# Performance work log

Measured on AMD Instinct MI355X. Metric: run time of the kernel, lower is better.

The kernel has to match this reference:

```python
import jax, jax.numpy as jnp
import numpy as np

NUM_HEADS = 4

def setup_inputs() -> dict:
    key = jax.random.key(0)
    ks = jax.random.split(key, 8)
    B, C, H, W = 4, 256, 128, 128
    Cq = C // 8  # query/key channels
    x  = jax.random.normal(ks[0], (B, C, H, W), dtype=jnp.float32)
    Wq = jax.random.normal(ks[1], (Cq, C), dtype=jnp.float32) * 0.05
    bq = jax.random.normal(ks[2], (Cq,),  dtype=jnp.float32) * 0.01
    Wk = jax.random.normal(ks[3], (Cq, C), dtype=jnp.float32) * 0.05
    bk = jax.random.normal(ks[4], (Cq,),  dtype=jnp.float32) * 0.01
    Wv = jax.random.normal(ks[5], (C, C),  dtype=jnp.float32) * 0.05
    bv = jax.random.normal(ks[6], (C,),   dtype=jnp.float32) * 0.01
    # torch init is zeros; use a nonzero value so the attention path contributes
    gamma = jnp.array([0.5], dtype=jnp.float32)
    return {"x": x, "Wq": Wq, "bq": bq, "Wk": Wk, "bk": bk, "Wv": Wv, "bv": bv, "gamma": gamma}

def _conv1x1(x, Wm, b):
    # 1x1 conv == per-pixel linear map over channels
    return jnp.einsum('bchw,oc->bohw', x, Wm) + b[None, :, None, None]

def reference(x, Wq, bq, Wk, bk, Wv, bv, gamma):
    B, C, H, W = x.shape
    nh = NUM_HEADS
    # project, then fold heads into batch: (B*nh, c_head, H, W)
    q = _conv1x1(x, Wq, bq).reshape(B * nh, -1, H, W)
    k = _conv1x1(x, Wk, bk).reshape(B * nh, -1, H, W)
    v = _conv1x1(x, Wv, bv).reshape(B * nh, -1, H, W)
    # horizontal (row-wise) attention over W: energy [BH, H, W, W]
    e_h = jnp.einsum('bchw,bchv->bhwv', q, k)
    a_h = jax.nn.softmax(e_h, axis=-1)
    o_h = jnp.einsum('bhwv,bchv->bchw', a_h, v)  # (BH, cv, H, W)
    # vertical (column-wise) attention over H: energy [BH, W, H, H]
    e_v = jnp.einsum('bchw,bcgw->bwhg', q, k)
    a_v = jax.nn.softmax(e_v, axis=-1)
    # original permutes back as (BH, cv, W, H); requires H == W to add
    o_v = jnp.einsum('bwhg,bcgw->bcwh', a_v, v)
    attn = (o_h + o_v).reshape(B, C, H, W)
    return gamma * attn + x
```

## Files before the change

kernel.cpp:

```cpp
#include <hip/hip_runtime.h>

#define HW 16384

typedef __attribute__((ext_vector_type(8))) short short8;
typedef __attribute__((ext_vector_type(16))) float floatx16;

__device__ inline unsigned short f2bf(float f) {
    unsigned u = __builtin_bit_cast(unsigned, f);
    u = (u + 0x7FFFu + ((u >> 16) & 1u)) >> 16;
    return (unsigned short)u;
}

__device__ inline unsigned pack_bf_trunc(float lo, float hi) {
    return __builtin_amdgcn_perm(__builtin_bit_cast(unsigned, hi),
                                 __builtin_bit_cast(unsigned, lo), 0x07060302u);
}

__global__ __launch_bounds__(256) void castW_kernel(
    const float* __restrict__ Wq, const float* __restrict__ Wk,
    const float* __restrict__ Wv, unsigned short* __restrict__ Wb)
{
    int idx4 = blockIdx.x * 256 + threadIdx.x;
    int e0 = idx4 * 4;
    int row = e0 >> 8, col = e0 & 255;
    const float* src = (row < 32) ? (Wq + row * 256 + col)
                     : (row < 64) ? (Wk + (row - 32) * 256 + col)
                                  : (Wv + (row - 64) * 256 + col);
    float4 v = *(const float4*)src;
    uint2 pk;
    pk.x = f2bf(v.x) | ((unsigned)f2bf(v.y) << 16);
    pk.y = f2bf(v.z) | ((unsigned)f2bf(v.w) << 16);
    *(uint2*)&Wb[e0] = pk;
}

__global__ __launch_bounds__(256) void cast_xt_kernel(
    const float* __restrict__ x, unsigned short* __restrict__ xt)
{
    __shared__ unsigned short T[64][66];
    const int tid = threadIdx.x;
    const int p0 = blockIdx.x * 64;
    const int c0 = blockIdx.y * 64;
    const int b  = blockIdx.z;
    #pragma unroll
    for (int i = 0; i < 4; i++) {
        int e = i * 256 + tid;
        int c = e >> 4, seg = e & 15;
        float4 v = *(const float4*)&x[((b * 256 + c0 + c) << 14) + p0 + seg * 4];
        ((unsigned*)&T[c][seg * 4])[0] = f2bf(v.x) | ((unsigned)f2bf(v.y) << 16);
        ((unsigned*)&T[c][seg * 4])[1] = f2bf(v.z) | ((unsigned)f2bf(v.w) << 16);
    }
    __syncthreads();
    #pragma unroll
    for (int i = 0; i < 2; i++) {
        int e = i * 256 + tid;
        int p = e >> 3, cs = e & 7;
        unsigned short t[8];
        #pragma unroll
        for (int j = 0; j < 8; j++) t[j] = T[cs * 8 + j][p];
        uint4 pk;
        pk.x = t[0] | ((unsigned)t[1] << 16);
        pk.y = t[2] | ((unsigned)t[3] << 16);
        pk.z = t[4] | ((unsigned)t[5] << 16);
        pk.w = t[6] | ((unsigned)t[7] << 16);
        *(uint4*)&xt[(((b << 14) + p0 + p) << 8) + c0 + cs * 8] = pk;
    }
}

__global__ __launch_bounds__(256, 3) void proj_mfma_kernel(
    const unsigned short* __restrict__ Wb, const unsigned short* __restrict__ xt,
    const float* __restrict__ bq, const float* __restrict__ bk,
    const float* __restrict__ bv,
    unsigned short* __restrict__ qb, unsigned short* __restrict__ kb,
    unsigned short* __restrict__ vb)
{
    __shared__ __align__(16) unsigned short As[64 * 64];
    __shared__ __align__(16) unsigned short Bs[256 * 64];
    __shared__ float biasS[64];
    const int tid = threadIdx.x;
    const int p0  = blockIdx.x * 256;
    const int oc0 = blockIdx.y * 64;
    const int b   = blockIdx.z;
    const int w = tid >> 6, lr = tid & 31, lh = (tid & 63) >> 5;

    if (tid < 64) biasS[tid] = (oc0 == 0) ? ((tid < 32) ? bq[tid] : bk[tid - 32])
                                          : bv[oc0 - 64 + tid];

    floatx16 z16 = {0,0,0,0,0,0,0,0,0,0,0,0,0,0,0,0};
    floatx16 acc[2][2] = {{z16, z16}, {z16, z16}};
    const int bpx = (b << 14) + p0;

    for (int kc = 0; kc < 256; kc += 64) {
        if (kc) __syncthreads();
        #pragma unroll
        for (int i = 0; i < 2; i++) {
            int e = i * 256 + tid;
            int row = e >> 3, seg = e & 7, cp = seg ^ (row & 7);
            *(uint4*)&As[row * 64 + cp * 8] =
                *(const uint4*)&Wb[(oc0 + row) * 256 + kc + seg * 8];
        }
        #pragma unroll
        for (int i = 0; i < 8; i++) {
            int e = i * 256 + tid;
            int row = e >> 3, seg = e & 7, cp = seg ^ (row & 7);
            *(uint4*)&Bs[row * 64 + cp * 8] =
                *(const uint4*)&xt[((bpx + row) << 8) + kc + seg * 8];
        }
        __syncthreads();
        #pragma unroll
        for (int ks = 0; ks < 4; ks++) {
            int c = 2 * ks + lh;
            int cx = (c ^ (lr & 7)) * 8;
            short8 af0 = *(const short8*)&As[lr * 64 + cx];
            short8 af1 = *(const short8*)&As[(32 + lr) * 64 + cx];
            short8 bf0 = *(const short8*)&Bs[(64 * w + lr) * 64 + cx];
            short8 bf1 = *(const short8*)&Bs[(64 * w + 32 + lr) * 64 + cx];
            acc[0][0] = __builtin_amdgcn_mfma_f32_32x32x16_bf16(af0, bf0, acc[0][0], 0, 0, 0);
            acc[0][1] = __builtin_amdgcn_mfma_f32_32x32x16_bf16(af0, bf1, acc[0][1], 0, 0, 0);
            acc[1][0] = __builtin_amdgcn_mfma_f32_32x32x16_bf16(af1, bf0, acc[1][0], 0, 0, 0);
            acc[1][1] = __builtin_amdgcn_mfma_f32_32x32x16_bf16(af1, bf1, acc[1][1], 0, 0, 0);
        }
    }

    __syncthreads();
    if (oc0 == 0) {
        unsigned short* Cq = Bs;
        #pragma unroll
        for (int i = 0; i < 2; i++) {
            #pragma unroll
            for (int j = 0; j < 2; j++) {
                int px = 64 * w + 32 * j + lr;
                #pragma unroll
                for (int g = 0; g < 4; g++) {
                    float v0 = acc[i][j][4*g+0] + biasS[32*i + 8*g + 4*lh + 0];
                    float v1 = acc[i][j][4*g+1] + biasS[32*i + 8*g + 4*lh + 1];
                    float v2 = acc[i][j][4*g+2] + biasS[32*i + 8*g + 4*lh + 2];
                    float v3 = acc[i][j][4*g+3] + biasS[32*i + 8*g + 4*lh + 3];
                    uint2 u; u.x = pack_bf_trunc(v0, v1); u.y = pack_bf_trunc(v2, v3);
                    int cp = (4 * i + g) ^ (px & 7);
                    *(uint2*)&Cq[px * 64 + cp * 8 + 4 * lh] = u;
                }
            }
        }
        __syncthreads();
        #pragma unroll
        for (int i = 0; i < 8; i++) {
            int px = tid;
            int cp = i ^ (px & 7);
            uint4 val = *(const uint4*)&Cq[px * 64 + cp * 8];
            if (i < 4) *(uint4*)&qb[(unsigned)((b * 4 + i)     * HW + p0 + px) * 8] = val;
            else       *(uint4*)&kb[(unsigned)((b * 4 + i - 4) * HW + p0 + px) * 8] = val;
        }
    } else {
        unsigned short* Cv = Bs;
        #pragma unroll
        for (int i = 0; i < 2; i++) {
            #pragma unroll
            for (int j = 0; j < 2; j++) {
                int px = 64 * w + 32 * j + lr;
                #pragma unroll
                for (int reg = 0; reg < 16; reg++) {
                    int oc = 32 * i + (reg & 3) + 8 * (reg >> 2) + 4 * lh;
                    float v = acc[i][j][reg] + biasS[oc];
                    int cp = (px >> 3) ^ (oc & 31);
                    Cv[oc * 256 + cp * 8 + (px & 7)] =
                        (unsigned short)(__builtin_bit_cast(unsigned, v) >> 16);
                }
            }
        }
        __syncthreads();
        #pragma unroll
        for (int i = 0; i < 8; i++) {
            int u = i * 256 + tid;
            int oc = u >> 5, seg = u & 31;
            int cp = seg ^ (oc & 31);
            uint4 val = *(const uint4*)&Cv[oc * 256 + cp * 8];
            *(uint4*)&vb[(unsigned)(b * 256 + oc0 - 64 + oc) * HW + p0 + seg * 8] = val;
        }
    }
}

__global__ __launch_bounds__(256) void tqk_kernel(
    const unsigned short* __restrict__ qb, const unsigned short* __restrict__ kb,
    unsigned short* __restrict__ qt, unsigned short* __restrict__ kt)
{
    __shared__ uint4 t[32][33];
    const int plane = blockIdx.y;
    const int tile  = blockIdx.x;
    const int tx = tile & 3, ty = tile >> 2;
    const uint4* src = (const uint4*)(plane < 16 ? qb : kb) + (plane & 15) * HW;
    uint4*       dst = (uint4*)(plane < 16 ? qt : kt) + (plane & 15) * HW;
    const int c = threadIdx.x & 31, r0 = threadIdx.x >> 5;
    #pragma unroll
    for (int i = 0; i < 4; i++) {
        int r = r0 + i * 8;
        t[r][c] = src[(ty * 32 + r) * 128 + tx * 32 + c];
    }
    __syncthreads();
    #pragma unroll
    for (int i = 0; i < 4; i++) {
        int r = r0 + i * 8;
        dst[(tx * 32 + r) * 128 + ty * 32 + c] = t[c][r];
    }
}

__global__ __launch_bounds__(256) void tv_kernel(
    const unsigned short* __restrict__ vb, unsigned short* __restrict__ vt)
{
    __shared__ unsigned short T[64][66];
    const int plane = blockIdx.y;
    const int tile  = blockIdx.x;
    const int tx = tile & 1, ty = tile >> 1;
    const unsigned* src = (const unsigned*)(vb + plane * HW);
    unsigned*       dst = (unsigned*)(vt + plane * HW);
    const int tid = threadIdx.x;
    #pragma unroll
    for (int i = 0; i < 8; i++) {
        int e = i * 256 + tid;
        int r = e >> 5, cp = e & 31;
        *(unsigned*)&T[r][2 * cp] = src[(ty * 64 + r) * 64 + tx * 32 + cp];
    }
    __syncthreads();
    #pragma unroll
    for (int i = 0; i < 8; i++) {
        int e = i * 256 + tid;
        int c = e >> 5, rp = e & 31;
        unsigned lo = T[2 * rp][c], hi = T[2 * rp + 1][c];
        dst[(tx * 64 + c) * 64 + ty * 32 + rp] = lo | (hi << 16);
    }
}

__global__ __launch_bounds__(256, 3) void attn_kernel(
    const unsigned short* __restrict__ qb, const unsigned short* __restrict__ kb,
    const unsigned short* __restrict__ vb,
    const unsigned short* __restrict__ qt, const unsigned short* __restrict__ kt,
    const unsigned short* __restrict__ vt,
    const float* __restrict__ xin, const float* __restrict__ gamma,
    float* __restrict__ out)
{
    __shared__ __align__(16) unsigned short Vs[64 * 128];
    __shared__ __align__(16) unsigned short Ps[128 * 128];
    __shared__ float red[4][128];

    const int tid = threadIdx.x;
    const int y = blockIdx.x, bh = blockIdx.y;
    const int w = tid >> 6, l = tid & 63, lr = l & 31, lh = l >> 5;
    const float L2E = 1.4426950408889634f;

    floatx16 z16 = {0,0,0,0,0,0,0,0,0,0,0,0,0,0,0,0};
    floatx16 o0 = z16, o1 = z16;
    short8 z8 = {0,0,0,0,0,0,0,0};

    for (int stage = 0; stage < 2; stage++) {
        const unsigned short* qsrc = (stage ? qt : qb) + (bh * 128 + y) * 1024;
        const unsigned short* ksrc = (stage ? kt : kb) + (bh * 128 + y) * 1024;
        const unsigned short* vsrc = stage ? vt : vb;
        if (stage) __syncthreads();
        #pragma unroll
        for (int i = 0; i < 4; i++) {
            int e = i * 256 + tid;
            int ch = e >> 4, sg = e & 15;
            int sgp = sg ^ (ch & 15);
            *(uint4*)&Vs[ch * 128 + sgp * 8] =
                *(const uint4*)(vsrc + (bh * 64 + ch) * HW + y * 128 + sg * 8);
        }
        short8 af = z8;
        short8 bf[4] = {z8, z8, z8, z8};
        if (lh == 0) {
            af = *(const short8*)(ksrc + (32 * w + lr) * 8);
            #pragma unroll
            for (int nt = 0; nt < 4; nt++)
                bf[nt] = *(const short8*)(qsrc + (32 * nt + lr) * 8);
        }
        floatx16 et[4];
        #pragma unroll
        for (int nt = 0; nt < 4; nt++)
            et[nt] = __builtin_amdgcn_mfma_f32_32x32x16_bf16(af, bf[nt], z16, 0, 0, 0);

        #pragma unroll
        for (int nt = 0; nt < 4; nt++) {
            float s = 0.f;
            #pragma unroll
            for (int r = 0; r < 16; r++) {
                float p = exp2f(et[nt][r] * L2E);
                et[nt][r] = p;
                s += p;
            }
            s += __shfl_xor(s, 32);
            if (lh == 0) red[w][32 * nt + lr] = s;
        }
        __syncthreads();
        float rl[4];
        #pragma unroll
        for (int nt = 0; nt < 4; nt++) {
            int q = 32 * nt + lr;
            rl[nt] = 1.0f / (red[0][q] + red[1][q] + red[2][q] + red[3][q]);
        }
        #pragma unroll
        for (int nt = 0; nt < 4; nt++) {
            int row = 32 * nt + lr;
            #pragma unroll
            for (int g = 0; g < 4; g++) {
                uint2 u;
                u.x = pack_bf_trunc(et[nt][4*g+0] * rl[nt], et[nt][4*g+1] * rl[nt]);
                u.y = pack_bf_trunc(et[nt][4*g+2] * rl[nt], et[nt][4*g+3] * rl[nt]);
                int cp = (4 * w + g) ^ (lr & 15);
                *(uint2*)&Ps[row * 128 + cp * 8 + 4 * lh] = u;
            }
        }
        __syncthreads();
        #pragma unroll
        for (int ks = 0; ks < 8; ks++) {
            int cp = ((2 * ks + lh) ^ (lr & 15)) * 8;
            short8 pf = *(const short8*)&Ps[(32 * w + lr) * 128 + cp];
            short8 v0 = *(const short8*)&Vs[lr * 128 + cp];
            short8 v1 = *(const short8*)&Vs[(32 + lr) * 128 + cp];
            o0 = __builtin_amdgcn_mfma_f32_32x32x16_bf16(v0, pf, o0, 0, 0, 0);
            o1 = __builtin_amdgcn_mfma_f32_32x32x16_bf16(v1, pf, o1, 0, 0, 0);
        }
    }

    const float g = gamma[0];
    const int xq = 32 * w + lr;
    #pragma unroll
    for (int reg = 0; reg < 16; reg++) {
        int ch = (reg & 3) + 8 * (reg >> 2) + 4 * lh;
        int idx0 = (bh * 64 + ch) * HW + y * 128 + xq;
        int idx1 = (bh * 64 + 32 + ch) * HW + y * 128 + xq;
        out[idx0] = g * o0[reg] + xin[idx0];
        out[idx1] = g * o1[reg] + xin[idx1];
    }
}

extern "C" void kernel_launch(void* const* d_in, const int* in_sizes, int n_in,
                              void* d_out, int out_size, void* d_ws, size_t ws_size,
                              hipStream_t stream) {
    const float* x     = (const float*)d_in[0];
    const float* Wq    = (const float*)d_in[1];
    const float* bq    = (const float*)d_in[2];
    const float* Wk    = (const float*)d_in[3];
    const float* bk    = (const float*)d_in[4];
    const float* Wv    = (const float*)d_in[5];
    const float* bv    = (const float*)d_in[6];
    const float* gamma = (const float*)d_in[7];
    float* out = (float*)d_out;

    unsigned short* Wb   = (unsigned short*)d_ws;
    unsigned short* qb16 = Wb + 320 * 256;
    unsigned short* kb16 = qb16 + 16 * HW * 8;
    unsigned short* qt16 = kb16 + 16 * HW * 8;
    unsigned short* kt16 = qt16 + 16 * HW * 8;
    unsigned short* vb16 = kt16 + 16 * HW * 8;
    unsigned short* vt16 = vb16 + 1024 * HW;
    unsigned short* xt = (unsigned short*)d_out;

    castW_kernel<<<dim3(80), 256, 0, stream>>>(Wq, Wk, Wv, Wb);
    cast_xt_kernel<<<dim3(256, 4, 4), 256, 0, stream>>>(x, xt);
    proj_mfma_kernel<<<dim3(64, 5, 4), 256, 0, stream>>>(Wb, xt, bq, bk, bv, qb16, kb16, vb16);
    tqk_kernel<<<dim3(16, 32), 256, 0, stream>>>(qb16, kb16, qt16, kt16);
    tv_kernel<<<dim3(4, 1024), 256, 0, stream>>>(vb16, vt16);
    attn_kernel<<<dim3(128, 16), 256, 0, stream>>>(qb16, kb16, vb16, qt16, kt16, vt16, x, gamma, out);
}
```

Baseline: 202.4 us.

## Restructure projection to stage x tile once, make attention register-resident

The projection kernel now loads a full 128-pixel x 256-channel tile of x into shared memory once. It loops over all five output-channel groups, reading weights directly from global memory, instead of launching a separate block per group that reloads x. The attention kernel computes energies transposed so each wave holds its own query columns. It builds the P operand in registers through lane shuffles instead of writing to shared memory, and drops the cross-wave softmax reduction barrier by deferring normalization (rescaling stage-0 output by the sum ratio). Both V tiles are preloaded up front. This trades shared-memory traffic and barriers for more registers, and changes occupancy targets on both kernels.

```diff
diff --git a/kernel.cpp b/kernel.cpp
--- a/kernel.cpp
+++ b/kernel.cpp
@@ -66,115 +66,103 @@
     }
 }
 
-__global__ __launch_bounds__(256, 3) void proj_mfma_kernel(
+__global__ __launch_bounds__(256, 2) void proj_mfma_kernel(
     const unsigned short* __restrict__ Wb, const unsigned short* __restrict__ xt,
     const float* __restrict__ bq, const float* __restrict__ bk,
     const float* __restrict__ bv,
     unsigned short* __restrict__ qb, unsigned short* __restrict__ kb,
     unsigned short* __restrict__ vb)
 {
-    __shared__ __align__(16) unsigned short As[64 * 64];
-    __shared__ __align__(16) unsigned short Bs[256 * 64];
-    __shared__ float biasS[64];
+    __shared__ __align__(16) unsigned short Bs[128 * 256];
+    __shared__ __align__(16) unsigned short Cs[32 * 128];
+    __shared__ float biasS[320];
     const int tid = threadIdx.x;
-    const int p0  = blockIdx.x * 256;
-    const int oc0 = blockIdx.y * 64;
-    const int b   = blockIdx.z;
+    const int p0  = blockIdx.x * 128;
+    const int b   = blockIdx.y;
     const int w = tid >> 6, lr = tid & 31, lh = (tid & 63) >> 5;
 
-    if (tid < 64) biasS[tid] = (oc0 == 0) ? ((tid < 32) ? bq[tid] : bk[tid - 32])
-                                          : bv[oc0 - 64 + tid];
+    if (tid < 64) biasS[tid] = (tid < 32) ? bq[tid] : bk[tid - 32];
+    biasS[64 + tid] = bv[tid];
+
+    const int bpx = (b << 14) + p0;
+    #pragma unroll
+    for (int i = 0; i < 16; i++) {
+        int e = i * 256 + tid;
+        int row = e >> 5, c = e & 31, cp = c ^ (row & 7);
+        *(uint4*)&Bs[row * 256 + cp * 8] =
+            *(const uint4*)&xt[(bpx + row) * 256 + c * 8];
+    }
+    __syncthreads();
 
     floatx16 z16 = {0,0,0,0,0,0,0,0,0,0,0,0,0,0,0,0};
-    floatx16 acc[2][2] = {{z16, z16}, {z16, z16}};
-    const int bpx = (b << 14) + p0;
-
-    for (int kc = 0; kc < 256; kc += 64) {
-        if (kc) __syncthreads();
-        #pragma unroll
-        for (int i = 0; i < 2; i++) {
-            int e = i * 256 + tid;
-            int row = e >> 3, seg = e & 7, cp = seg ^ (row & 7);
-            *(uint4*)&As[row * 64 + cp * 8] =
-                *(const uint4*)&Wb[(oc0 + row) * 256 + kc + seg * 8];
-        }
-        #pragma unroll
-        for (int i = 0; i < 8; i++) {
-            int e = i * 256 + tid;
-            int row = e >> 3, seg = e & 7, cp = seg ^ (row & 7);
-            *(uint4*)&Bs[row * 64 + cp * 8] =
-                *(const uint4*)&xt[((bpx + row) << 8) + kc + seg * 8];
-        }
-        __syncthreads();
-        #pragma unroll
-        for (int ks = 0; ks < 4; ks++) {
-            int c = 2 * ks + lh;
-            int cx = (c ^ (lr & 7)) * 8;
-            short8 af0 = *(const short8*)&As[lr * 64 + cx];
-            short8 af1 = *(const short8*)&As[(32 + lr) * 64 + cx];
-            short8 bf0 = *(const short8*)&Bs[(64 * w + lr) * 64 + cx];
-            short8 bf1 = *(const short8*)&Bs[(64 * w + 32 + lr) * 64 + cx];
-            acc[0][0] = __builtin_amdgcn_mfma_f32_32x32x16_bf16(af0, bf0, acc[0][0], 0, 0, 0);
-            acc[0][1] = __builtin_amdgcn_mfma_f32_32x32x16_bf16(af0, bf1, acc[0][1], 0, 0, 0);
-            acc[1][0] = __builtin_amdgcn_mfma_f32_32x32x16_bf16(af1, bf0, acc[1][0], 0, 0, 0);
-            acc[1][1] = __builtin_amdgcn_mfma_f32_32x32x16_bf16(af1, bf1, acc[1][1], 0, 0, 0);
-        }
-    }
-
-    __syncthreads();
-    if (oc0 == 0) {
-        unsigned short* Cq = Bs;
-        #pragma unroll
-        for (int i = 0; i < 2; i++) {
-            #pragma unroll
-            for (int j = 0; j < 2; j++) {
-                int px = 64 * w + 32 * j + lr;
+    const int brow = 32 * w + lr;
+
+    for (int ocg = 0; ocg < 5; ocg++) {
+        const int oc0 = ocg * 64;
+        floatx16 acc[2] = {z16, z16};
+        const unsigned short* wrow0 = Wb + (oc0 + lr) * 256 + 8 * lh;
+        const unsigned short* wrow1 = Wb + (oc0 + 32 + lr) * 256 + 8 * lh;
+        #pragma unroll
+        for (int ks = 0; ks < 16; ks++) {
+            short8 af0 = *(const short8*)(wrow0 + 16 * ks);
+            short8 af1 = *(const short8*)(wrow1 + 16 * ks);
+            int cpk = ((2 * ks + lh) ^ (brow & 7)) * 8;
+            short8 bfr = *(const short8*)&Bs[brow * 256 + cpk];
+            acc[0] = __builtin_amdgcn_mfma_f32_32x32x16_bf16(af0, bfr, acc[0], 0, 0, 0);
+            acc[1] = __builtin_amdgcn_mfma_f32_32x32x16_bf16(af1, bfr, acc[1], 0, 0, 0);
+        }
+
+        if (ocg == 0) {
+            #pragma unroll
+            for (int i = 0; i < 2; i++) {
+                int px = 32 * w + lr;
                 #pragma unroll
                 for (int g = 0; g < 4; g++) {
-                    float v0 = acc[i][j][4*g+0] + biasS[32*i + 8*g + 4*lh + 0];
-                    float v1 = acc[i][j][4*g+1] + biasS[32*i + 8*g + 4*lh + 1];
-                    float v2 = acc[i][j][4*g+2] + biasS[32*i + 8*g + 4*lh + 2];
-                    float v3 = acc[i][j][4*g+3] + biasS[32*i + 8*g + 4*lh + 3];
+                    float v0 = acc[i][4*g+0] + biasS[32*i + 8*g + 4*lh + 0];
+                    float v1 = acc[i][4*g+1] + biasS[32*i + 8*g + 4*lh + 1];
+                    float v2 = acc[i][4*g+2] + biasS[32*i + 8*g + 4*lh + 2];
+                    float v3 = acc[i][4*g+3] + biasS[32*i + 8*g + 4*lh + 3];
                     uint2 u; u.x = pack_bf_trunc(v0, v1); u.y = pack_bf_trunc(v2, v3);
-                    int cp = (4 * i + g) ^ (px & 7);
-                    *(uint2*)&Cq[px * 64 + cp * 8 + 4 * lh] = u;
+                    int cp = g ^ (px & 3);
+                    *(uint2*)&Cs[px * 32 + cp * 8 + 4 * lh] = u;
                 }
+                __syncthreads();
+                #pragma unroll
+                for (int i2 = 0; i2 < 2; i2++) {
+                    int u4 = i2 * 256 + tid;
+                    int hl = u4 >> 7, px2 = u4 & 127;
+                    int cp = hl ^ (px2 & 3);
+                    uint4 val = *(const uint4*)&Cs[px2 * 32 + cp * 8];
+                    unsigned off = (unsigned)((b * 4 + hl) * HW + p0 + px2) * 8;
+                    if (i == 0) *(uint4*)&qb[off] = val;
+                    else        *(uint4*)&kb[off] = val;
+                }
+                __syncthreads();
             }
-        }
-        __syncthreads();
-        #pragma unroll
-        for (int i = 0; i < 8; i++) {
-            int px = tid;
-            int cp = i ^ (px & 7);
-            uint4 val = *(const uint4*)&Cq[px * 64 + cp * 8];
-            if (i < 4) *(uint4*)&qb[(unsigned)((b * 4 + i)     * HW + p0 + px) * 8] = val;
-            else       *(uint4*)&kb[(unsigned)((b * 4 + i - 4) * HW + p0 + px) * 8] = val;
-        }
-    } else {
-        unsigned short* Cv = Bs;
-        #pragma unroll
-        for (int i = 0; i < 2; i++) {
-            #pragma unroll
-            for (int j = 0; j < 2; j++) {
-                int px = 64 * w + 32 * j + lr;
+        } else {
+            #pragma unroll
+            for (int i = 0; i < 2; i++) {
+                int px = 32 * w + lr;
                 #pragma unroll
                 for (int reg = 0; reg < 16; reg++) {
-                    int oc = 32 * i + (reg & 3) + 8 * (reg >> 2) + 4 * lh;
-                    float v = acc[i][j][reg] + biasS[oc];
-                    int cp = (px >> 3) ^ (oc & 31);
-                    Cv[oc * 256 + cp * 8 + (px & 7)] =
+                    int m = (reg & 3) + 8 * (reg >> 2) + 4 * lh;
+                    float v = acc[i][reg] + biasS[oc0 + 32 * i + m];
+                    int cp = (px >> 3) ^ (m & 15);
+                    Cs[m * 128 + cp * 8 + (px & 7)] =
                         (unsigned short)(__builtin_bit_cast(unsigned, v) >> 16);
                 }
+                __syncthreads();
+                #pragma unroll
+                for (int i2 = 0; i2 < 2; i2++) {
+                    int u4 = i2 * 256 + tid;
+                    int m = u4 >> 4, seg = u4 & 15;
+                    int cp = seg ^ (m & 15);
+                    uint4 val = *(const uint4*)&Cs[m * 128 + cp * 8];
+                    *(uint4*)&vb[(unsigned)((b * 256 + oc0 - 64 + 32 * i + m) * HW
+                                            + p0 + seg * 8)] = val;
+                }
+                __syncthreads();
             }
-        }
-        __syncthreads();
-        #pragma unroll
-        for (int i = 0; i < 8; i++) {
-            int u = i * 256 + tid;
-            int oc = u >> 5, seg = u & 31;
-            int cp = seg ^ (oc & 31);
-            uint4 val = *(const uint4*)&Cv[oc * 256 + cp * 8];
-            *(uint4*)&vb[(unsigned)(b * 256 + oc0 - 64 + oc) * HW + p0 + seg * 8] = val;
         }
     }
 }
@@ -229,7 +217,7 @@
     }
 }
 
-__global__ __launch_bounds__(256, 3) void attn_kernel(
+__global__ __launch_bounds__(256, 4) void attn_kernel(
     const unsigned short* __restrict__ qb, const unsigned short* __restrict__ kb,
     const unsigned short* __restrict__ vb,
     const unsigned short* __restrict__ qt, const unsigned short* __restrict__ kt,
@@ -237,97 +225,96 @@
     const float* __restrict__ xin, const float* __restrict__ gamma,
     float* __restrict__ out)
 {
-    __shared__ __align__(16) unsigned short Vs[64 * 128];
-    __shared__ __align__(16) unsigned short Ps[128 * 128];
-    __shared__ float red[4][128];
+    __shared__ __align__(16) unsigned short Vs[2][64 * 128];
 
     const int tid = threadIdx.x;
     const int y = blockIdx.x, bh = blockIdx.y;
     const int w = tid >> 6, l = tid & 63, lr = l & 31, lh = l >> 5;
     const float L2E = 1.4426950408889634f;
 
+    #pragma unroll
+    for (int s = 0; s < 2; s++) {
+        const unsigned short* vsrc = s ? vt : vb;
+        #pragma unroll
+        for (int i = 0; i < 4; i++) {
+            int e = i * 256 + tid;
+            int ch = e >> 4, sg = e & 15, sgp = sg ^ (ch & 15);
+            *(uint4*)&Vs[s][ch * 128 + sgp * 8] =
+                *(const uint4*)(vsrc + (bh * 64 + ch) * HW + y * 128 + sg * 8);
+        }
+    }
+    __syncthreads();
+
     floatx16 z16 = {0,0,0,0,0,0,0,0,0,0,0,0,0,0,0,0};
     floatx16 o0 = z16, o1 = z16;
     short8 z8 = {0,0,0,0,0,0,0,0};
-
+    float s0s = 1.0f;
+
+    #pragma unroll
     for (int stage = 0; stage < 2; stage++) {
         const unsigned short* qsrc = (stage ? qt : qb) + (bh * 128 + y) * 1024;
         const unsigned short* ksrc = (stage ? kt : kb) + (bh * 128 + y) * 1024;
-        const unsigned short* vsrc = stage ? vt : vb;
-        if (stage) __syncthreads();
-        #pragma unroll
-        for (int i = 0; i < 4; i++) {
-            int e = i * 256 + tid;
-            int ch = e >> 4, sg = e & 15;
-            int sgp = sg ^ (ch & 15);
-            *(uint4*)&Vs[ch * 128 + sgp * 8] =
-                *(const uint4*)(vsrc + (bh * 64 + ch) * HW + y * 128 + sg * 8);
-        }
-        short8 af = z8;
-        short8 bf[4] = {z8, z8, z8, z8};
-        if (lh == 0) {
-            af = *(const short8*)(ksrc + (32 * w + lr) * 8);
-            #pragma unroll
-            for (int nt = 0; nt < 4; nt++)
-                bf[nt] = *(const short8*)(qsrc + (32 * nt + lr) * 8);
-        }
-        floatx16 et[4];
-        #pragma unroll
-        for (int nt = 0; nt < 4; nt++)
-            et[nt] = __builtin_amdgcn_mfma_f32_32x32x16_bf16(af, bf[nt], z16, 0, 0, 0);
-
-        #pragma unroll
-        for (int nt = 0; nt < 4; nt++) {
-            float s = 0.f;
+        short8 bf = z8;
+        if (lh == 0) bf = *(const short8*)(qsrc + (32 * w + lr) * 8);
+
+        float partial = 0.f;
+        short8 pf[8];
+        #pragma unroll
+        for (int kg = 0; kg < 4; kg++) {
+            short8 af = z8;
+            if (lh == 0) af = *(const short8*)(ksrc + (32 * kg + lr) * 8);
+            floatx16 e = __builtin_amdgcn_mfma_f32_32x32x16_bf16(af, bf, z16, 0, 0, 0);
             #pragma unroll
             for (int r = 0; r < 16; r++) {
-                float p = exp2f(et[nt][r] * L2E);
-                et[nt][r] = p;
-                s += p;
+                float p = exp2f(e[r] * L2E);
+                e[r] = p;
+                partial += p;
             }
-            s += __shfl_xor(s, 32);
-            if (lh == 0) red[w][32 * nt + lr] = s;
-        }
-        __syncthreads();
-        float rl[4];
-        #pragma unroll
-        for (int nt = 0; nt < 4; nt++) {
-            int q = 32 * nt + lr;
-            rl[nt] = 1.0f / (red[0][q] + red[1][q] + red[2][q] + red[3][q]);
-        }
-        #pragma unroll
-        for (int nt = 0; nt < 4; nt++) {
-            int row = 32 * nt + lr;
-            #pragma unroll
-            for (int g = 0; g < 4; g++) {
-                uint2 u;
-                u.x = pack_bf_trunc(et[nt][4*g+0] * rl[nt], et[nt][4*g+1] * rl[nt]);
-                u.y = pack_bf_trunc(et[nt][4*g+2] * rl[nt], et[nt][4*g+3] * rl[nt]);
-                int cp = (4 * w + g) ^ (lr & 15);
-                *(uint2*)&Ps[row * 128 + cp * 8 + 4 * lh] = u;
+            #pragma unroll
+            for (int cc = 0; cc < 2; cc++) {
+                unsigned X0 = pack_bf_trunc(e[8*cc+0], e[8*cc+1]);
+                unsigned X1 = pack_bf_trunc(e[8*cc+2], e[8*cc+3]);
+                unsigned X2 = pack_bf_trunc(e[8*cc+4], e[8*cc+5]);
+                unsigned X3 = pack_bf_trunc(e[8*cc+6], e[8*cc+7]);
+                unsigned pX0 = __shfl_xor(X0, 32);
+                unsigned pX1 = __shfl_xor(X1, 32);
+                unsigned pX2 = __shfl_xor(X2, 32);
+                unsigned pX3 = __shfl_xor(X3, 32);
+                union { unsigned u[4]; short8 s8; } t;
+                t.u[0] = lh ? pX2 : X0;
+                t.u[1] = lh ? pX3 : X1;
+                t.u[2] = lh ? X2  : pX0;
+                t.u[3] = lh ? X3  : pX1;
+                pf[2 * kg + cc] = t.s8;
             }
         }
-        __syncthreads();
+        float ssum = partial + __shfl_xor(partial, 32);
+        if (stage == 1) {
+            float f = ssum / s0s;
+            #pragma unroll
+            for (int r = 0; r < 16; r++) { o0[r] *= f; o1[r] *= f; }
+        }
+        s0s = ssum;
+
         #pragma unroll
         for (int ks = 0; ks < 8; ks++) {
             int cp = ((2 * ks + lh) ^ (lr & 15)) * 8;
-            short8 pf = *(const short8*)&Ps[(32 * w + lr) * 128 + cp];
-            short8 v0 = *(const short8*)&Vs[lr * 128 + cp];
-            short8 v1 = *(const short8*)&Vs[(32 + lr) * 128 + cp];
-            o0 = __builtin_amdgcn_mfma_f32_32x32x16_bf16(v0, pf, o0, 0, 0, 0);
-            o1 = __builtin_amdgcn_mfma_f32_32x32x16_bf16(v1, pf, o1, 0, 0, 0);
-        }
-    }
-
-    const float g = gamma[0];
+            short8 v0 = *(const short8*)&Vs[stage][lr * 128 + cp];
+            short8 v1 = *(const short8*)&Vs[stage][(32 + lr) * 128 + cp];
+            o0 = __builtin_amdgcn_mfma_f32_32x32x16_bf16(v0, pf[ks], o0, 0, 0, 0);
+            o1 = __builtin_amdgcn_mfma_f32_32x32x16_bf16(v1, pf[ks], o1, 0, 0, 0);
+        }
+    }
+
+    const float gs = gamma[0] / s0s;
     const int xq = 32 * w + lr;
     #pragma unroll
     for (int reg = 0; reg < 16; reg++) {
         int ch = (reg & 3) + 8 * (reg >> 2) + 4 * lh;
         int idx0 = (bh * 64 + ch) * HW + y * 128 + xq;
         int idx1 = (bh * 64 + 32 + ch) * HW + y * 128 + xq;
-        out[idx0] = g * o0[reg] + xin[idx0];
-        out[idx1] = g * o1[reg] + xin[idx1];
+        out[idx0] = gs * o0[reg] + xin[idx0];
+        out[idx1] = gs * o1[reg] + xin[idx1];
     }
 }
 
@@ -355,7 +342,7 @@
 
     castW_kernel<<<dim3(80), 256, 0, stream>>>(Wq, Wk, Wv, Wb);
     cast_xt_kernel<<<dim3(256, 4, 4), 256, 0, stream>>>(x, xt);
-    proj_mfma_kernel<<<dim3(64, 5, 4), 256, 0, stream>>>(Wb, xt, bq, bk, bv, qb16, kb16, vb16);
+    proj_mfma_kernel<<<dim3(128, 4), 256, 0, stream>>>(Wb, xt, bq, bk, bv, qb16, kb16, vb16);
     tqk_kernel<<<dim3(16, 32), 256, 0, stream>>>(qb16, kb16, qt16, kt16);
     tv_kernel<<<dim3(4, 1024), 256, 0, stream>>>(vb16, vt16);
     attn_kernel<<<dim3(128, 16), 256, 0, stream>>>(qb16, kb16, vb16, qt16, kt16, vt16, x, gamma, out);
```

Result: slower. 253.3 us (+25.1%).
